# Performance work log

Hardware: AMD Instinct MI355X
Metric: run time of the kernel (lower is better)

Reference implementation:

```python
import jax, jax.numpy as jnp
import numpy as np

DIM = 2048
NH = 16
HD = DIM // NH
B = 2
S = 2048
HID = 5632  # multiple_of*ceil(int(2*4*dim/3)/multiple_of)
EPS = 1e-6


def setup_inputs() -> dict:
    key = jax.random.key(0)
    ks = jax.random.split(key, 9)
    sd = 0.02
    x = jax.random.normal(ks[0], (B, S, DIM), jnp.float32)
    wq = jax.random.normal(ks[1], (DIM, DIM), jnp.float32) * sd
    wk = jax.random.normal(ks[2], (DIM, DIM), jnp.float32) * sd
    wv = jax.random.normal(ks[3], (DIM, DIM), jnp.float32) * sd
    wo = jax.random.normal(ks[4], (DIM, DIM), jnp.float32) * sd
    w1 = jax.random.normal(ks[5], (DIM, HID), jnp.float32) * sd
    w2 = jax.random.normal(ks[6], (HID, DIM), jnp.float32) * sd
    w3 = jax.random.normal(ks[7], (DIM, HID), jnp.float32) * sd
    attn_norm_w = jnp.ones((DIM,), jnp.float32)
    ffn_norm_w = jnp.ones((DIM,), jnp.float32)
    # RoPE tables: freqs_cis = exp(i * t * theta_j), theta_j = 10000^(-2j/HD)
    inv_freq = 1.0 / (10000.0 ** (np.arange(0, HD, 2).astype(np.float32) / HD))
    t = np.arange(S, dtype=np.float32)
    ang = np.outer(t, inv_freq)  # [S, HD/2]
    freqs_cos = jnp.asarray(np.cos(ang), jnp.float32)
    freqs_sin = jnp.asarray(np.sin(ang), jnp.float32)
    # causal additive mask [1,1,S,S]
    mask = jnp.triu(jnp.full((S, S), float('-inf'), jnp.float32), k=1)[None, None]
    return dict(x=x, wq=wq, wk=wk, wv=wv, wo=wo, w1=w1, w2=w2, w3=w3,
                attn_norm_w=attn_norm_w, ffn_norm_w=ffn_norm_w,
                freqs_cos=freqs_cos, freqs_sin=freqs_sin, mask=mask)


def _rmsnorm(x, w):
    xf = x.astype(jnp.float32)
    v = jnp.mean(xf * xf, axis=-1, keepdims=True)
    return (xf * jax.lax.rsqrt(v + EPS)).astype(x.dtype) * w


def _rope(t, cos, sin):
    # t: [B,S,H,HD] -> pairs (re, im) on last dim
    tr = t.reshape(*t.shape[:-1], HD // 2, 2)
    re, im = tr[..., 0], tr[..., 1]
    c = cos[None, :, None, :]
    s = sin[None, :, None, :]
    out_re = re * c - im * s
    out_im = re * s + im * c
    return jnp.stack([out_re, out_im], axis=-1).reshape(t.shape)


def reference(x, wq, wk, wv, wo, w1, w2, w3, attn_norm_w, ffn_norm_w,
              freqs_cos, freqs_sin, mask):
    # --- attention sublayer ---
    h_in = _rmsnorm(x, attn_norm_w)
    xq = (h_in @ wq).reshape(B, S, NH, HD)
    xk = (h_in @ wk).reshape(B, S, NH, HD)
    xv = (h_in @ wv).reshape(B, S, NH, HD)
    xq = _rope(xq, freqs_cos, freqs_sin)
    xk = _rope(xk, freqs_cos, freqs_sin)
    scale = 1.0 / jnp.sqrt(jnp.float32(HD))
    scores = jnp.einsum('bqhd,bkhd->bhqk', xq, xk) * scale + mask
    probs = jax.nn.softmax(scores.astype(jnp.float32), axis=-1).astype(xq.dtype)
    attn = jnp.einsum('bhqk,bkhd->bqhd', probs, xv).reshape(B, S, DIM)
    h = x + attn @ wo
    # --- feedforward sublayer (SwiGLU) ---
    f_in = _rmsnorm(h, ffn_norm_w)
    ffn = (jax.nn.silu(f_in @ w1) * (f_in @ w3)) @ w2
    return h + ffn
```

## Files before the change

kernel.cpp:

```cpp
#include <hip/hip_runtime.h>

#define DIMQ 2048
#define NHQ  16
#define HDQ  128
#define BQ   2
#define SQ   2048
#define HIDQ 5632
#define MQ   (BQ * SQ)
#define SC_ATTN 0.08838834764831845f

using u16 = unsigned short;
using u32 = unsigned int;
typedef __attribute__((ext_vector_type(8))) short s16x8;
typedef __attribute__((ext_vector_type(4))) float f32x4;

__device__ __forceinline__ float bf2f(u16 v) {
  union { u32 u; float f; } w; w.u = ((u32)v) << 16; return w.f;
}
__device__ __forceinline__ u16 f2bf(float f) {
  union { float f; u32 u; } w; w.f = f;
  u32 r = w.u + 0x7FFFu + ((w.u >> 16) & 1u);
  return (u16)(r >> 16);
}

__device__ __forceinline__ f32x4 mfma16(s16x8 a, s16x8 b, f32x4 c) {
  return __builtin_amdgcn_mfma_f32_16x16x32_bf16(a, b, c, 0, 0, 0);
}

__device__ __forceinline__ void gl_lds16(const void* g, void* l) {
  __builtin_amdgcn_global_load_lds((const __attribute__((address_space(1))) void*)g,
                                   (__attribute__((address_space(3))) void*)l,
                                   16, 0, 0);
}

#define SBAR()                                   \
  {                                              \
    asm volatile("" ::: "memory");               \
    __builtin_amdgcn_s_barrier();                \
    asm volatile("" ::: "memory");               \
  }

__global__ __launch_bounds__(256) void transpose_cvt(const float* __restrict__ src,
                                                     u16* __restrict__ dst,
                                                     int R, int Cn) {
  __shared__ float tile[32][33];
  const int tx = threadIdx.x, ty = threadIdx.y;
  const int c0 = blockIdx.x * 32, r0 = blockIdx.y * 32;
#pragma unroll
  for (int i = 0; i < 4; ++i)
    tile[ty + i * 8][tx] = src[(size_t)(r0 + ty + i * 8) * Cn + c0 + tx];
  __syncthreads();
#pragma unroll
  for (int i = 0; i < 4; ++i)
    dst[(size_t)(c0 + ty + i * 8) * R + r0 + tx] = f2bf(tile[tx][ty + i * 8]);
}

__global__ __launch_bounds__(256) void transpose_cvt_ffn(const float* __restrict__ src,
                                                         u16* __restrict__ dst,
                                                         int base) {
  __shared__ float tile[32][33];
  const int tx = threadIdx.x, ty = threadIdx.y;
  const int c0 = blockIdx.x * 32, r0 = blockIdx.y * 32;
#pragma unroll
  for (int i = 0; i < 4; ++i)
    tile[ty + i * 8][tx] = src[(size_t)(r0 + ty + i * 8) * HIDQ + c0 + tx];
  __syncthreads();
#pragma unroll
  for (int i = 0; i < 4; ++i) {
    const int n = c0 + ty + i * 8;
    const int row = (n >> 7) * 256 + base + (n & 127);
    dst[(size_t)row * DIMQ + r0 + tx] = f2bf(tile[tx][ty + i * 8]);
  }
}

__global__ __launch_bounds__(256) void vtrans_k(const u16* __restrict__ qkv,
                                                u16* __restrict__ vt) {
  __shared__ u16 tile[32][33];
  const int bh = blockIdx.z;
  const int b = bh >> 4, h = bh & 15;
  const int s0 = blockIdx.x * 32, d0 = blockIdx.y * 32;
  const int tx = threadIdx.x, ty = threadIdx.y;
  const u16* src = qkv + (size_t)(b * SQ) * 6144 + 4096 + h * HDQ;
#pragma unroll
  for (int i = 0; i < 4; ++i)
    tile[ty + i * 8][tx] = src[(size_t)(s0 + ty + i * 8) * 6144 + d0 + tx];
  __syncthreads();
  u16* dst = vt + (size_t)bh * HDQ * SQ;
#pragma unroll
  for (int i = 0; i < 4; ++i)
    dst[(size_t)(d0 + ty + i * 8) * SQ + s0 + tx] = tile[tx][ty + i * 8];
}

__global__ __launch_bounds__(256) void rmsnorm_k(const float* __restrict__ x,
                                                 const float* __restrict__ w,
                                                 u16* __restrict__ o) {
  const int row = blockIdx.x;
  const int t = threadIdx.x;
  const float* xr = x + (size_t)row * DIMQ;
  const float4 a = ((const float4*)xr)[t * 2];
  const float4 b = ((const float4*)xr)[t * 2 + 1];
  float ss = a.x * a.x + a.y * a.y + a.z * a.z + a.w * a.w +
             b.x * b.x + b.y * b.y + b.z * b.z + b.w * b.w;
#pragma unroll
  for (int off = 32; off > 0; off >>= 1) ss += __shfl_down(ss, off);
  __shared__ float red[4];
  if ((t & 63) == 0) red[t >> 6] = ss;
  __syncthreads();
  ss = red[0] + red[1] + red[2] + red[3];
  const float rs = rsqrtf(ss * (1.0f / (float)DIMQ) + 1e-6f);
  const float4 wa = ((const float4*)w)[t * 2];
  const float4 wb = ((const float4*)w)[t * 2 + 1];
  s16x8 ov;
  ov[0] = (short)f2bf(a.x * rs * wa.x);
  ov[1] = (short)f2bf(a.y * rs * wa.y);
  ov[2] = (short)f2bf(a.z * rs * wa.z);
  ov[3] = (short)f2bf(a.w * rs * wa.w);
  ov[4] = (short)f2bf(b.x * rs * wb.x);
  ov[5] = (short)f2bf(b.y * rs * wb.y);
  ov[6] = (short)f2bf(b.z * rs * wb.z);
  ov[7] = (short)f2bf(b.w * rs * wb.w);
  *(s16x8*)(o + (size_t)row * DIMQ + t * 8) = ov;
}

template <int OM, int BN, int ROPE>
__global__ __launch_bounds__(512, 1) void gemm256(const u16* __restrict__ A,
                                                  const u16* __restrict__ Bt,
                                                  u16* __restrict__ Cb,
                                                  float* __restrict__ Cf,
                                                  const float* __restrict__ resid,
                                                  const float* __restrict__ fc,
                                                  const float* __restrict__ fs,
                                                  int N, int K, int lda) {
  constexpr int BT = BN * 128;
  constexpr int BLB = BN / 128;
  constexpr int WNv = (BN == 256) ? 4 : 2;
  constexpr int MF = (BN == 256) ? 8 : 4;
  constexpr int MFH = MF / 2;
  __shared__ u16 lds[(65536 + 2 * BT) / 2];
  const int tid = threadIdx.x, wid = tid >> 6, lane = tid & 63;
  const int wm = wid / WNv, wn = wid % WNv;
  const int r = lane & 15, kc = lane >> 4;
  const int nbx = N / BN;
  const int nwg = nbx << 4;
  const int o = blockIdx.x;
  const int seq = (o & 7) * (nwg >> 3) + (o >> 3);
  const int by = seq / nbx, bx = seq - by * nbx;
  const int m0 = by << 8, n0 = bx * BN;
  const int T = K >> 6;

  const u16* Ag = A + (size_t)m0 * lda;
  const u16* Bg = Bt + (size_t)n0 * K;

  const int pl = (tid * 16) ^ (((tid >> 3) & 7) << 4);
  const int prow = pl >> 7;
  const int pcol = (pl & 127) >> 1;

  const int rd0 = r * 128 + ((kc * 16) ^ ((r & 7) << 4));
  const int waveA = wm * (MF * 2048);
  const int waveB = wn * 8192;

  f32x4 acc[MF][4] = {};
  s16x8 af[MFH][2], bfL[2][2], bfH[2][2];

#define STAGE_A(G, kt, BUFB, h)                                                   \
  {                                                                               \
    _Pragma("unroll") for (int i = 0; i < 2; ++i)                                 \
        gl_lds16(G + (size_t)((h) * 128 + i * 64 + prow) * lda + (kt) * 64 + pcol,\
                 (char*)lds + (BUFB) + (h) * 16384 + i * 8192 + (wid << 10));     \
  }
#define STAGE_B(G, kt, BUFB, h)                                                   \
  {                                                                               \
    _Pragma("unroll") for (int i = 0; i < BLB; ++i)                               \
        gl_lds16(G + (size_t)((h) * (BN / 2) + i * 64 + prow) * K + (kt) * 64 + pcol, \
                 (char*)lds + (BUFB) + (h) * (BT / 2) + i * 8192 + (wid << 10));  \
  }

  STAGE_A(Ag, 0, 0, 0);
  STAGE_A(Ag, 0, 0, 1);
  STAGE_B(Bg, 0, 65536, 0);
  STAGE_B(Bg, 0, 65536, 1);
  STAGE_A(Ag, 1, 32768, 0);
  STAGE_A(Ag, 1, 32768, 1);
  asm volatile("s_waitcnt vmcnt(4)" ::: "memory");
  SBAR();

#define TILE_BODY(t, cur)                                                         \
  {                                                                               \
    const int tp1 = ((t) + 1 < T) ? (t) + 1 : T - 1;                              \
    const int tp2 = ((t) + 2 < T) ? (t) + 2 : T - 1;                              \
    const int AB = (cur)*32768;                                                   \
    const int BB = 65536 + (cur)*BT;                                              \
    const int BBn = 65536 + (1 - (cur)) * BT;                                     \
           \
    STAGE_B(Bg, tp1, BBn, 0);                                                     \
    _Pragma("unroll") for (int j = 0; j < MFH; ++j)                               \
        _Pragma("unroll") for (int ks = 0; ks < 2; ++ks)                          \
            af[j][ks] = *(const s16x8*)((const char*)lds + AB + waveA +           \
                                        j * 2048 + (rd0 ^ (ks << 6)));            \
    _Pragma("unroll") for (int n = 0; n < 2; ++n)                                 \
        _Pragma("unroll") for (int ks = 0; ks < 2; ++ks)                          \
            bfL[n][ks] = *(const s16x8*)((const char*)lds + BB + waveB +          \
                                         n * 2048 + (rd0 ^ (ks << 6)));           \
    __builtin_amdgcn_s_setprio(1);                                                \
    _Pragma("unroll") for (int ks = 0; ks < 2; ++ks)                              \
        _Pragma("unroll") for (int j = 0; j < MFH; ++j)                           \
            _Pragma("unroll") for (int n = 0; n < 2; ++n)                         \
                acc[j][n] = mfma16(af[j][ks], bfL[n][ks], acc[j][n]);             \
    __builtin_amdgcn_s_setprio(0);                                                \
                 \
    STAGE_B(Bg, tp1, BBn, 1);                                                     \
    _Pragma("unroll") for (int n = 0; n < 2; ++n)                                 \
        _Pragma("unroll") for (int ks = 0; ks < 2; ++ks)                          \
            bfH[n][ks] = *(const s16x8*)((const char*)lds + BB + waveB +          \
                                         (2 + n) * 2048 + (rd0 ^ (ks << 6)));     \
    __builtin_amdgcn_s_setprio(1);                                                \
    _Pragma("unroll") for (int ks = 0; ks < 2; ++ks)                              \
        _Pragma("unroll") for (int j = 0; j < MFH; ++j)                           \
            _Pragma("unroll") for (int n = 0; n < 2; ++n)                         \
                acc[j][2 + n] = mfma16(af[j][ks], bfH[n][ks], acc[j][2 + n]);     \
    __builtin_amdgcn_s_setprio(0);                                                \
                                  \
    _Pragma("unroll") for (int j = 0; j < MFH; ++j)                               \
        _Pragma("unroll") for (int ks = 0; ks < 2; ++ks)                          \
            af[j][ks] = *(const s16x8*)((const char*)lds + AB + waveA +           \
                                        (MFH + j) * 2048 + (rd0 ^ (ks << 6)));    \
    __builtin_amdgcn_s_setprio(1);                                                \
    _Pragma("unroll") for (int ks = 0; ks < 2; ++ks)                              \
        _Pragma("unroll") for (int j = 0; j < MFH; ++j)                           \
            _Pragma("unroll") for (int n = 0; n < 2; ++n)                         \
                acc[MFH + j][n] = mfma16(af[j][ks], bfL[n][ks], acc[MFH + j][n]); \
    __builtin_amdgcn_s_setprio(0);                                                \
    SBAR();     \
                  \
    STAGE_A(Ag, tp2, AB, 0);                                                      \
    STAGE_A(Ag, tp2, AB, 1);                                                      \
    __builtin_amdgcn_s_setprio(1);                                                \
    _Pragma("unroll") for (int ks = 0; ks < 2; ++ks)                              \
        _Pragma("unroll") for (int j = 0; j < MFH; ++j)                           \
            _Pragma("unroll") for (int n = 0; n < 2; ++n)                         \
                acc[MFH + j][2 + n] = mfma16(af[j][ks], bfH[n][ks], acc[MFH + j][2 + n]); \
    __builtin_amdgcn_s_setprio(0);                                                \
    asm volatile("s_waitcnt vmcnt(4)" ::: "memory");    \
    SBAR();                                                                       \
  }

  for (int tt = 0; tt < T; tt += 2) {
    TILE_BODY(tt, 0);
    TILE_BODY(tt + 1, 1);
  }
#undef TILE_BODY
#undef STAGE_A
#undef STAGE_B

  const bool do_rope = ROPE && (n0 < 4096);
#pragma unroll
  for (int mf = 0; mf < MF; ++mf)
#pragma unroll
    for (int nf = 0; nf < 4; ++nf)
#pragma unroll
      for (int j = 0; j < 4; ++j) {
        const int rr = m0 + wm * (MF * 16) + mf * 16 + kc * 4 + j;
        const int cc = n0 + wn * 64 + nf * 16 + r;
        float v = acc[mf][nf][j];
        if (OM == 0) {
          if (ROPE) {
            const float partner = __shfl_xor(v, 1);
            if (do_rope) {
              const int s = rr & (SQ - 1);
              const int i0 = (cc >> 1) & 63;
              const float cv = fc[s * 64 + i0];
              const float sv = fs[s * 64 + i0];
              v = ((r & 1) == 0) ? v * cv - partner * sv : v * cv + partner * sv;
            }
          }
          Cb[(size_t)rr * N + cc] = f2bf(v);
        } else {
          Cf[(size_t)rr * N + cc] = v + resid[(size_t)rr * N + cc];
        }
      }
}

__global__ __launch_bounds__(512, 1) void gemm_ffn(const u16* __restrict__ A,
                                                   const u16* __restrict__ Bi,
                                                   u16* __restrict__ act) {
  __shared__ u16 lds[65536];
  const int tid = threadIdx.x, wid = tid >> 6, lane = tid & 63;
  const int wm = wid >> 1, wn = wid & 1;
  const int r = lane & 15, kc = lane >> 4;
  const int o = blockIdx.x;
  const int seq = (o & 7) * 88 + (o >> 3);
  const int by = seq / 44, bx = seq - by * 44;
  const int m0 = by << 8;
  const int T = 32;

  const u16* Ag = A + (size_t)m0 * DIMQ;
  const u16* Bg = Bi + (size_t)bx * 256 * DIMQ;

  const int pl = (tid * 16) ^ (((tid >> 3) & 7) << 4);
  const int prow = pl >> 7, pcol = (pl & 127) >> 1;
  const int rd0 = r * 128 + ((kc * 16) ^ ((r & 7) << 4));
  const int waveA = wm * 8192;
  const int waveB = wn * 8192;

  f32x4 accG[4][4] = {}, accU[4][4] = {};
  s16x8 af[4][2], bL[2][2], bH[2][2];

#define STG(G, kt, BUFB, h)                                                       \
  {                                                                               \
    _Pragma("unroll") for (int i = 0; i < 2; ++i)                                 \
        gl_lds16(G + (size_t)((h) * 128 + i * 64 + prow) * DIMQ + (kt) * 64 + pcol,\
                 (char*)lds + (BUFB) + (h) * 16384 + i * 8192 + (wid << 10));     \
  }

  STG(Ag, 0, 0, 0);
  STG(Ag, 0, 0, 1);
  STG(Bg, 0, 65536, 0);
  STG(Bg, 0, 65536, 1);
  STG(Ag, 1, 32768, 0);
  STG(Ag, 1, 32768, 1);
  asm volatile("s_waitcnt vmcnt(4)" ::: "memory");
  SBAR();

#define FFN_BODY(t, cur)                                                          \
  {                                                                               \
    const int tp1 = ((t) + 1 < T) ? (t) + 1 : T - 1;                              \
    const int tp2 = ((t) + 2 < T) ? (t) + 2 : T - 1;                              \
    const int AB = (cur)*32768;                                                   \
    const int BB = 65536 + (cur)*32768;                                           \
    const int BBn = 65536 + (1 - (cur)) * 32768;                                  \
                            \
    STG(Bg, tp1, BBn, 0);                                                         \
    _Pragma("unroll") for (int j = 0; j < 4; ++j)                                 \
        _Pragma("unroll") for (int ks = 0; ks < 2; ++ks)                          \
            af[j][ks] = *(const s16x8*)((const char*)lds + AB + waveA +           \
                                        j * 2048 + (rd0 ^ (ks << 6)));            \
    _Pragma("unroll") for (int n = 0; n < 2; ++n)                                 \
        _Pragma("unroll") for (int ks = 0; ks < 2; ++ks)                          \
            bL[n][ks] = *(const s16x8*)((const char*)lds + BB + waveB +           \
                                        n * 2048 + (rd0 ^ (ks << 6)));            \
    __builtin_amdgcn_s_setprio(1);                                                \
    _Pragma("unroll") for (int ks = 0; ks < 2; ++ks)                              \
        _Pragma("unroll") for (int j = 0; j < 4; ++j)                             \
            _Pragma("unroll") for (int n = 0; n < 2; ++n)                         \
                accG[j][n] = mfma16(af[j][ks], bL[n][ks], accG[j][n]);            \
    __builtin_amdgcn_s_setprio(0);                                                \
                                 \
    STG(Bg, tp1, BBn, 1);                                                         \
    _Pragma("unroll") for (int n = 0; n < 2; ++n)                                 \
        _Pragma("unroll") for (int ks = 0; ks < 2; ++ks)                          \
            bH[n][ks] = *(const s16x8*)((const char*)lds + BB + waveB +           \
                                        (2 + n) * 2048 + (rd0 ^ (ks << 6)));      \
    __builtin_amdgcn_s_setprio(1);                                                \
    _Pragma("unroll") for (int ks = 0; ks < 2; ++ks)                              \
        _Pragma("unroll") for (int j = 0; j < 4; ++j)                             \
            _Pragma("unroll") for (int n = 0; n < 2; ++n)                         \
                accG[j][2 + n] = mfma16(af[j][ks], bH[n][ks], accG[j][2 + n]);    \
    __builtin_amdgcn_s_setprio(0);                                                \
                                                    \
    _Pragma("unroll") for (int n = 0; n < 2; ++n)                                 \
        _Pragma("unroll") for (int ks = 0; ks < 2; ++ks)                          \
            bL[n][ks] = *(const s16x8*)((const char*)lds + BB + 16384 + waveB +   \
                                        n * 2048 + (rd0 ^ (ks << 6)));            \
    __builtin_amdgcn_s_setprio(1);                                                \
    _Pragma("unroll") for (int ks = 0; ks < 2; ++ks)                              \
        _Pragma("unroll") for (int j = 0; j < 4; ++j)                             \
            _Pragma("unroll") for (int n = 0; n < 2; ++n)                         \
                accU[j][n] = mfma16(af[j][ks], bL[n][ks], accU[j][n]);            \
    __builtin_amdgcn_s_setprio(0);                                                \
                                                             \
    _Pragma("unroll") for (int n = 0; n < 2; ++n)                                 \
        _Pragma("unroll") for (int ks = 0; ks < 2; ++ks)                          \
            bH[n][ks] = *(const s16x8*)((const char*)lds + BB + 16384 + waveB +   \
                                        (2 + n) * 2048 + (rd0 ^ (ks << 6)));      \
    SBAR();                        \
                                                 \
    STG(Ag, tp2, AB, 0);                                                          \
    STG(Ag, tp2, AB, 1);                                                          \
    __builtin_amdgcn_s_setprio(1);                                                \
    _Pragma("unroll") for (int ks = 0; ks < 2; ++ks)                              \
        _Pragma("unroll") for (int j = 0; j < 4; ++j)                             \
            _Pragma("unroll") for (int n = 0; n < 2; ++n)                         \
                accU[j][2 + n] = mfma16(af[j][ks], bH[n][ks], accU[j][2 + n]);    \
    __builtin_amdgcn_s_setprio(0);                                                \
    asm volatile("s_waitcnt vmcnt(4)" ::: "memory");                              \
    SBAR();                                                                       \
  }

  for (int tt = 0; tt < T; tt += 2) {
    FFN_BODY(tt, 0);
    FFN_BODY(tt + 1, 1);
  }
#undef FFN_BODY
#undef STG

  const int cbase = bx * 128 + wn * 64;
#pragma unroll
  for (int mf = 0; mf < 4; ++mf)
#pragma unroll
    for (int nf = 0; nf < 4; ++nf)
#pragma unroll
      for (int j = 0; j < 4; ++j) {
        const int rr = m0 + wm * 64 + mf * 16 + kc * 4 + j;
        const int cc = cbase + nf * 16 + r;
        const float g = accG[mf][nf][j];
        const float u = accU[mf][nf][j];
        const float a = g / (1.f + __expf(-g)) * u;
        act[(size_t)rr * HIDQ + cc] = f2bf(a);
      }
}

__global__ __launch_bounds__(512) void attn_k(const u16* __restrict__ qkv,
                                              const u16* __restrict__ vt,
                                              u16* __restrict__ outb) {
  __shared__ u16 Kl[64 * 136];
  __shared__ u16 Vl[128 * 72];
  __shared__ u16 Pl[8][16 * 80];
  const int bh = blockIdx.x;
  const int pr = blockIdx.y;
  const int b = bh >> 4, h = bh & 15;
  const int tid = threadIdx.x, wid = tid >> 6, lane = tid & 63;
  const int r = lane & 15, kc = lane >> 4;
  const int nt_lo = pr + 1, nt = 32 - pr;
  const int qbase = ((wid < 4) ? pr * 64 : (31 - pr) * 64) + (wid & 3) * 16;
  const size_t base = (size_t)b * SQ * 6144;
  const u16* vtb = vt + (size_t)bh * HDQ * SQ;
  s16x8 qf[4];
  {
    const size_t qoff = base + (size_t)(qbase + r) * 6144 + h * HDQ;
#pragma unroll
    for (int kk = 0; kk < 4; ++kk)
      qf[kk] = *(const s16x8*)&qkv[qoff + kk * 32 + kc * 8];
  }
  f32x4 acc_o[8] = {};
  float m_run[4], l_run[4];
#pragma unroll
  for (int j = 0; j < 4; ++j) { m_run[j] = -1e30f; l_run[j] = 0.f; }
  const int kr = tid >> 4, kc8 = (tid & 15) * 8;
  const int vr = tid >> 3, vc8 = (tid & 7) * 8;
  const u16* kgp = &qkv[base + (size_t)kr * 6144 + 2048 + h * HDQ + kc8];
  const u16* vgp = &vtb[(size_t)vr * SQ + vc8];
  s16x8 kreg[2], vreg[2];
  kreg[0] = *(const s16x8*)kgp;
  kreg[1] = *(const s16x8*)(kgp + (size_t)32 * 6144);
  vreg[0] = *(const s16x8*)vgp;
  vreg[1] = *(const s16x8*)(vgp + (size_t)64 * SQ);
  for (int t = 0; t < nt; ++t) {
    const int kv0 = t * 64;
    __syncthreads();
    *(s16x8*)&Kl[kr * 136 + kc8] = kreg[0];
    *(s16x8*)&Kl[(kr + 32) * 136 + kc8] = kreg[1];
    *(s16x8*)&Vl[vr * 72 + vc8] = vreg[0];
    *(s16x8*)&Vl[(vr + 64) * 72 + vc8] = vreg[1];
    __syncthreads();
    if (t + 1 < nt) {
      const u16* kg = kgp + (size_t)(kv0 + 64) * 6144;
      const u16* vg = vgp + (kv0 + 64);
      kreg[0] = *(const s16x8*)kg;
      kreg[1] = *(const s16x8*)(kg + (size_t)32 * 6144);
      vreg[0] = *(const s16x8*)vg;
      vreg[1] = *(const s16x8*)(vg + (size_t)64 * SQ);
    }
    if (wid >= 4 || t < nt_lo) {
      f32x4 sacc[4] = {};
      __builtin_amdgcn_s_setprio(1);
#pragma unroll
      for (int nf = 0; nf < 4; ++nf)
#pragma unroll
        for (int kk = 0; kk < 4; ++kk) {
          const s16x8 kf = *(const s16x8*)&Kl[(nf * 16 + r) * 136 + kk * 32 + kc * 8];
          sacc[nf] = mfma16(qf[kk], kf, sacc[nf]);
        }
      __builtin_amdgcn_s_setprio(0);
      float p[4][4], alpha[4];
#pragma unroll
      for (int j = 0; j < 4; ++j) {
        const int qrow = qbase + kc * 4 + j;
        float svs[4];
        float tm = -1e30f;
#pragma unroll
        for (int nf = 0; nf < 4; ++nf) {
          const int key = kv0 + nf * 16 + r;
          float sv = sacc[nf][j] * SC_ATTN;
          sv = (key > qrow) ? -1e30f : sv;
          svs[nf] = sv;
          tm = fmaxf(tm, sv);
        }
        tm = fmaxf(tm, __shfl_xor(tm, 1));
        tm = fmaxf(tm, __shfl_xor(tm, 2));
        tm = fmaxf(tm, __shfl_xor(tm, 4));
        tm = fmaxf(tm, __shfl_xor(tm, 8));
        const float mnew = fmaxf(m_run[j], tm);
        alpha[j] = __expf(m_run[j] - mnew);
        m_run[j] = mnew;
        float rs = 0.f;
#pragma unroll
        for (int nf = 0; nf < 4; ++nf) {
          const float pv = __expf(svs[nf] - mnew);
          p[nf][j] = pv;
          rs += pv;
        }
        rs += __shfl_xor(rs, 1);
        rs += __shfl_xor(rs, 2);
        rs += __shfl_xor(rs, 4);
        rs += __shfl_xor(rs, 8);
        l_run[j] = l_run[j] * alpha[j] + rs;
      }
#pragma unroll
      for (int nf = 0; nf < 8; ++nf)
#pragma unroll
        for (int j = 0; j < 4; ++j)
          acc_o[nf][j] *= alpha[j];
#pragma unroll
      for (int nf = 0; nf < 4; ++nf)
#pragma unroll
        for (int j = 0; j < 4; ++j)
          Pl[wid][(kc * 4 + j) * 80 + nf * 16 + r] = f2bf(p[nf][j]);
      __builtin_amdgcn_s_setprio(1);
#pragma unroll
      for (int ks = 0; ks < 2; ++ks) {
        const s16x8 pa = *(const s16x8*)&Pl[wid][r * 80 + ks * 32 + kc * 8];
#pragma unroll
        for (int nf = 0; nf < 8; ++nf) {
          const s16x8 bv = *(const s16x8*)&Vl[(nf * 16 + r) * 72 + ks * 32 + kc * 8];
          acc_o[nf] = mfma16(pa, bv, acc_o[nf]);
        }
      }
      __builtin_amdgcn_s_setprio(0);
    }
  }
#pragma unroll
  for (int j = 0; j < 4; ++j) {
    const float inv = 1.0f / l_run[j];
    const size_t orow = (size_t)(b * SQ + qbase + kc * 4 + j) * DIMQ + h * HDQ;
#pragma unroll
    for (int nf = 0; nf < 8; ++nf)
      outb[orow + nf * 16 + r] = f2bf(acc_o[nf][j] * inv);
  }
}

extern "C" void kernel_launch(void* const* d_in, const int* in_sizes, int n_in,
                              void* d_out, int out_size, void* d_ws, size_t ws_size,
                              hipStream_t stream) {
  const float* x   = (const float*)d_in[0];
  const float* wq  = (const float*)d_in[1];
  const float* wk  = (const float*)d_in[2];
  const float* wv  = (const float*)d_in[3];
  const float* wo  = (const float*)d_in[4];
  const float* w1  = (const float*)d_in[5];
  const float* w2  = (const float*)d_in[6];
  const float* w3  = (const float*)d_in[7];
  const float* anw = (const float*)d_in[8];
  const float* fnw = (const float*)d_in[9];
  const float* fc  = (const float*)d_in[10];
  const float* fs  = (const float*)d_in[11];
  float* out = (float*)d_out;

  char* ws = (char*)d_ws;
  u16* wqkvT = (u16*)(ws);
  u16* woT   = (u16*)(ws + 25165824);
  u16* w13i  = (u16*)(ws + 25165824 + 8388608);
  u16* w2T   = (u16*)(ws + 25165824 + 8388608 + 46137344);
  u16* hin   = (u16*)(ws + 102760448);
  u16* qkvb  = (u16*)(ws + 119537664);
  u16* act   = qkvb;
  u16* attnb = (u16*)(ws + 119537664 + 50331648);
  u16* vtb   = (u16*)(ws + 119537664 + 50331648 + 16777216);
  float* h = out;

  const dim3 tb(32, 8);
  transpose_cvt<<<dim3(64, 64), tb, 0, stream>>>(wq, wqkvT, 2048, 2048);
  transpose_cvt<<<dim3(64, 64), tb, 0, stream>>>(wk, wqkvT + (size_t)2048 * 2048, 2048, 2048);
  transpose_cvt<<<dim3(64, 64), tb, 0, stream>>>(wv, wqkvT + (size_t)2 * 2048 * 2048, 2048, 2048);
  transpose_cvt<<<dim3(64, 64), tb, 0, stream>>>(wo, woT, 2048, 2048);
  transpose_cvt_ffn<<<dim3(176, 64), tb, 0, stream>>>(w1, w13i, 0);
  transpose_cvt_ffn<<<dim3(176, 64), tb, 0, stream>>>(w3, w13i, 128);
  transpose_cvt<<<dim3(64, 176), tb, 0, stream>>>(w2, w2T, 5632, 2048);

  rmsnorm_k<<<4096, 256, 0, stream>>>(x, anw, hin);
  gemm256<0, 128, 1><<<768, 512, 0, stream>>>(hin, wqkvT, qkvb, nullptr, nullptr, fc, fs, 6144, 2048, 2048);
  vtrans_k<<<dim3(64, 4, 32), tb, 0, stream>>>(qkvb, vtb);
  attn_k<<<dim3(32, 16), 512, 0, stream>>>(qkvb, vtb, attnb);
  gemm256<1, 128, 0><<<256, 512, 0, stream>>>(attnb, woT, nullptr, h, x, nullptr, nullptr, 2048, 2048, 2048);
  rmsnorm_k<<<4096, 256, 0, stream>>>(h, fnw, hin);
  gemm_ffn<<<704, 512, 0, stream>>>(hin, w13i, act);
  gemm256<1, 128, 0><<<256, 512, 0, stream>>>(act, w2T, nullptr, out, h, nullptr, nullptr, 2048, 5632, 5632);
}
```

Measured before the change: 633.7 us.

## Prefetch B tiles two iterations ahead alongside A in GEMM pipelines

Changes the B-operand staging in the generic GEMM and FFN GEMM kernels from one tile ahead to two tiles ahead, matching A. B loads are issued after the mid-tile barrier into the buffer just consumed, with an explicit lgkmcnt(0) wait added before that barrier, and the vmcnt waits are relaxed to keep more loads in flight. The aim is to hide global-load latency for B more fully. The cost is more outstanding memory operations and a dependence on the LDS reads finishing before the buffer is overwritten.

```diff
diff --git a/kernel.cpp b/kernel.cpp
--- a/kernel.cpp
+++ b/kernel.cpp
@@ -39,6 +39,7 @@
     __builtin_amdgcn_s_barrier();                \
     asm volatile("" ::: "memory");               \
   }
+#define LGKM0() asm volatile("s_waitcnt lgkmcnt(0)" ::: "memory")
 
 __global__ __launch_bounds__(256) void transpose_cvt(const float* __restrict__ src,
                                                      u16* __restrict__ dst,
@@ -174,6 +175,11 @@
         gl_lds16(G + (size_t)((h) * (BN / 2) + i * 64 + prow) * K + (kt) * 64 + pcol, \
                  (char*)lds + (BUFB) + (h) * (BT / 2) + i * 8192 + (wid << 10));  \
   }
+#define VMCNT_TILE()                                                              \
+  {                                                                               \
+    if (BN == 128) { asm volatile("s_waitcnt vmcnt(6)" ::: "memory"); }           \
+    else { asm volatile("s_waitcnt vmcnt(8)" ::: "memory"); }                     \
+  }
 
   STAGE_A(Ag, 0, 0, 0);
   STAGE_A(Ag, 0, 0, 1);
@@ -181,18 +187,17 @@
   STAGE_B(Bg, 0, 65536, 1);
   STAGE_A(Ag, 1, 32768, 0);
   STAGE_A(Ag, 1, 32768, 1);
-  asm volatile("s_waitcnt vmcnt(4)" ::: "memory");
+  STAGE_B(Bg, 1, 65536 + BT, 0);
+  STAGE_B(Bg, 1, 65536 + BT, 1);
+  VMCNT_TILE();
   SBAR();
 
 #define TILE_BODY(t, cur)                                                         \
   {                                                                               \
-    const int tp1 = ((t) + 1 < T) ? (t) + 1 : T - 1;                              \
     const int tp2 = ((t) + 2 < T) ? (t) + 2 : T - 1;                              \
     const int AB = (cur)*32768;                                                   \
     const int BB = 65536 + (cur)*BT;                                              \
-    const int BBn = 65536 + (1 - (cur)) * BT;                                     \
-           \
-    STAGE_B(Bg, tp1, BBn, 0);                                                     \
+                            \
     _Pragma("unroll") for (int j = 0; j < MFH; ++j)                               \
         _Pragma("unroll") for (int ks = 0; ks < 2; ++ks)                          \
             af[j][ks] = *(const s16x8*)((const char*)lds + AB + waveA +           \
@@ -207,8 +212,7 @@
             _Pragma("unroll") for (int n = 0; n < 2; ++n)                         \
                 acc[j][n] = mfma16(af[j][ks], bfL[n][ks], acc[j][n]);             \
     __builtin_amdgcn_s_setprio(0);                                                \
-                 \
-    STAGE_B(Bg, tp1, BBn, 1);                                                     \
+                                  \
     _Pragma("unroll") for (int n = 0; n < 2; ++n)                                 \
         _Pragma("unroll") for (int ks = 0; ks < 2; ++ks)                          \
             bfH[n][ks] = *(const s16x8*)((const char*)lds + BB + waveB +          \
@@ -230,17 +234,20 @@
             _Pragma("unroll") for (int n = 0; n < 2; ++n)                         \
                 acc[MFH + j][n] = mfma16(af[j][ks], bfL[n][ks], acc[MFH + j][n]); \
     __builtin_amdgcn_s_setprio(0);                                                \
-    SBAR();     \
-                  \
+    LGKM0();                             \
+    SBAR();                        \
+             \
     STAGE_A(Ag, tp2, AB, 0);                                                      \
     STAGE_A(Ag, tp2, AB, 1);                                                      \
+    STAGE_B(Bg, tp2, BB, 0);                                                      \
+    STAGE_B(Bg, tp2, BB, 1);                                                      \
     __builtin_amdgcn_s_setprio(1);                                                \
     _Pragma("unroll") for (int ks = 0; ks < 2; ++ks)                              \
         _Pragma("unroll") for (int j = 0; j < MFH; ++j)                           \
             _Pragma("unroll") for (int n = 0; n < 2; ++n)                         \
                 acc[MFH + j][2 + n] = mfma16(af[j][ks], bfH[n][ks], acc[MFH + j][2 + n]); \
     __builtin_amdgcn_s_setprio(0);                                                \
-    asm volatile("s_waitcnt vmcnt(4)" ::: "memory");    \
+    VMCNT_TILE();                 \
     SBAR();                                                                       \
   }
 
@@ -251,6 +258,7 @@
 #undef TILE_BODY
 #undef STAGE_A
 #undef STAGE_B
+#undef VMCNT_TILE
 
   const bool do_rope = ROPE && (n0 < 4096);
 #pragma unroll
@@ -318,18 +326,17 @@
   STG(Bg, 0, 65536, 1);
   STG(Ag, 1, 32768, 0);
   STG(Ag, 1, 32768, 1);
-  asm volatile("s_waitcnt vmcnt(4)" ::: "memory");
+  STG(Bg, 1, 98304, 0);
+  STG(Bg, 1, 98304, 1);
+  asm volatile("s_waitcnt vmcnt(8)" ::: "memory");
   SBAR();
 
 #define FFN_BODY(t, cur)                                                          \
   {                                                                               \
-    const int tp1 = ((t) + 1 < T) ? (t) + 1 : T - 1;                              \
     const int tp2 = ((t) + 2 < T) ? (t) + 2 : T - 1;                              \
     const int AB = (cur)*32768;                                                   \
     const int BB = 65536 + (cur)*32768;                                           \
-    const int BBn = 65536 + (1 - (cur)) * 32768;                                  \
-                            \
-    STG(Bg, tp1, BBn, 0);                                                         \
+                                            \
     _Pragma("unroll") for (int j = 0; j < 4; ++j)                                 \
         _Pragma("unroll") for (int ks = 0; ks < 2; ++ks)                          \
             af[j][ks] = *(const s16x8*)((const char*)lds + AB + waveA +           \
@@ -344,8 +351,7 @@
             _Pragma("unroll") for (int n = 0; n < 2; ++n)                         \
                 accG[j][n] = mfma16(af[j][ks], bL[n][ks], accG[j][n]);            \
     __builtin_amdgcn_s_setprio(0);                                                \
-                                 \
-    STG(Bg, tp1, BBn, 1);                                                         \
+                                                 \
     _Pragma("unroll") for (int n = 0; n < 2; ++n)                                 \
         _Pragma("unroll") for (int ks = 0; ks < 2; ++ks)                          \
             bH[n][ks] = *(const s16x8*)((const char*)lds + BB + waveB +           \
@@ -356,7 +362,7 @@
             _Pragma("unroll") for (int n = 0; n < 2; ++n)                         \
                 accG[j][2 + n] = mfma16(af[j][ks], bH[n][ks], accG[j][2 + n]);    \
     __builtin_amdgcn_s_setprio(0);                                                \
-                                                    \
+                                       \
     _Pragma("unroll") for (int n = 0; n < 2; ++n)                                 \
         _Pragma("unroll") for (int ks = 0; ks < 2; ++ks)                          \
             bL[n][ks] = *(const s16x8*)((const char*)lds + BB + 16384 + waveB +   \
@@ -367,22 +373,24 @@
             _Pragma("unroll") for (int n = 0; n < 2; ++n)                         \
                 accU[j][n] = mfma16(af[j][ks], bL[n][ks], accU[j][n]);            \
     __builtin_amdgcn_s_setprio(0);                                                \
-                                                             \
     _Pragma("unroll") for (int n = 0; n < 2; ++n)                                 \
         _Pragma("unroll") for (int ks = 0; ks < 2; ++ks)                          \
             bH[n][ks] = *(const s16x8*)((const char*)lds + BB + 16384 + waveB +   \
                                         (2 + n) * 2048 + (rd0 ^ (ks << 6)));      \
-    SBAR();                        \
-                                                 \
+    LGKM0();                    \
+    SBAR();                                                                       \
+                                 \
     STG(Ag, tp2, AB, 0);                                                          \
     STG(Ag, tp2, AB, 1);                                                          \
+    STG(Bg, tp2, BB, 0);                                                          \
+    STG(Bg, tp2, BB, 1);                                                          \
     __builtin_amdgcn_s_setprio(1);                                                \
     _Pragma("unroll") for (int ks = 0; ks < 2; ++ks)                              \
         _Pragma("unroll") for (int j = 0; j < 4; ++j)                             \
             _Pragma("unroll") for (int n = 0; n < 2; ++n)                         \
                 accU[j][2 + n] = mfma16(af[j][ks], bH[n][ks], accU[j][2 + n]);    \
     __builtin_amdgcn_s_setprio(0);                                                \
-    asm volatile("s_waitcnt vmcnt(4)" ::: "memory");                              \
+    asm volatile("s_waitcnt vmcnt(8)" ::: "memory");                              \
     SBAR();                                                                       \
   }
 
```

Result: slower. 649.5 us (+2.5%).

## Restructure attention softmax with transposed scores, exp2, lazy rescale, packed bf16 stores

Applied to the files above, without the earlier changes.

Computes the scores transposed (K·Q^T), so each lane holds one query row. Row max and sum then take two cross-lane shuffles instead of four per row, and only one running max/sum per lane is kept. The softmax scale and log2(e) are folded into Q at load time so exp2f can be used. Rescaling of the output accumulator is skipped unless the max grows by more than a threshold of 8. P is converted with packed v_cvt_pk_bf16 and written as 8-byte LDS stores. In exchange, Q is rounded to bf16 a second time after scaling, and the lazy-rescale threshold allows unnormalised exponentials up to 2^8, which could slightly change accuracy.

```diff
diff --git a/kernel.cpp b/kernel.cpp
--- a/kernel.cpp
+++ b/kernel.cpp
@@ -13,6 +13,7 @@
 using u32 = unsigned int;
 typedef __attribute__((ext_vector_type(8))) short s16x8;
 typedef __attribute__((ext_vector_type(4))) float f32x4;
+typedef __attribute__((ext_vector_type(2))) u32 u32x2;
 
 __device__ __forceinline__ float bf2f(u16 v) {
   union { u32 u; float f; } w; w.u = ((u32)v) << 16; return w.f;
@@ -21,6 +22,11 @@
   union { float f; u32 u; } w; w.f = f;
   u32 r = w.u + 0x7FFFu + ((w.u >> 16) & 1u);
   return (u16)(r >> 16);
+}
+__device__ __forceinline__ u32 cvtpk_bf16(float a, float b) {
+  u32 r;
+  asm("v_cvt_pk_bf16_f32 %0, %1, %2" : "=v"(r) : "v"(a), "v"(b));
+  return r;
 }
 
 __device__ __forceinline__ f32x4 mfma16(s16x8 a, s16x8 b, f32x4 c) {
@@ -39,6 +45,7 @@
     __builtin_amdgcn_s_barrier();                \
     asm volatile("" ::: "memory");               \
   }
+#define LGKM0() asm volatile("s_waitcnt lgkmcnt(0)" ::: "memory")
 
 __global__ __launch_bounds__(256) void transpose_cvt(const float* __restrict__ src,
                                                      u16* __restrict__ dst,
@@ -367,7 +374,7 @@
             _Pragma("unroll") for (int n = 0; n < 2; ++n)                         \
                 accU[j][n] = mfma16(af[j][ks], bL[n][ks], accU[j][n]);            \
     __builtin_amdgcn_s_setprio(0);                                                \
-                                                             \
+          \
     _Pragma("unroll") for (int n = 0; n < 2; ++n)                                 \
         _Pragma("unroll") for (int ks = 0; ks < 2; ++ks)                          \
             bH[n][ks] = *(const s16x8*)((const char*)lds + BB + 16384 + waveB +   \
@@ -422,19 +429,23 @@
   const int r = lane & 15, kc = lane >> 4;
   const int nt_lo = pr + 1, nt = 32 - pr;
   const int qbase = ((wid < 4) ? pr * 64 : (31 - pr) * 64) + (wid & 3) * 16;
+  const int qrow_r = qbase + r;
   const size_t base = (size_t)b * SQ * 6144;
   const u16* vtb = vt + (size_t)bh * HDQ * SQ;
   s16x8 qf[4];
   {
-    const size_t qoff = base + (size_t)(qbase + r) * 6144 + h * HDQ;
-#pragma unroll
-    for (int kk = 0; kk < 4; ++kk)
-      qf[kk] = *(const s16x8*)&qkv[qoff + kk * 32 + kc * 8];
+    const size_t qoff = base + (size_t)qrow_r * 6144 + h * HDQ;
+    const float QSC = SC_ATTN * 1.44269504f;
+#pragma unroll
+    for (int kk = 0; kk < 4; ++kk) {
+      s16x8 v = *(const s16x8*)&qkv[qoff + kk * 32 + kc * 8];
+#pragma unroll
+      for (int e = 0; e < 8; ++e) v[e] = (short)f2bf(bf2f((u16)v[e]) * QSC);
+      qf[kk] = v;
+    }
   }
   f32x4 acc_o[8] = {};
-  float m_run[4], l_run[4];
-#pragma unroll
-  for (int j = 0; j < 4; ++j) { m_run[j] = -1e30f; l_run[j] = 0.f; }
+  float m_run = -1e30f, l_run = 0.f;
   const int kr = tid >> 4, kc8 = (tid & 15) * 8;
   const int vr = tid >> 3, vc8 = (tid & 7) * 8;
   const u16* kgp = &qkv[base + (size_t)kr * 6144 + 2048 + h * HDQ + kc8];
@@ -461,60 +472,64 @@
       vreg[1] = *(const s16x8*)(vg + (size_t)64 * SQ);
     }
     if (wid >= 4 || t < nt_lo) {
-      f32x4 sacc[4] = {};
+      f32x4 st[4] = {};
       __builtin_amdgcn_s_setprio(1);
 #pragma unroll
       for (int nf = 0; nf < 4; ++nf)
 #pragma unroll
         for (int kk = 0; kk < 4; ++kk) {
           const s16x8 kf = *(const s16x8*)&Kl[(nf * 16 + r) * 136 + kk * 32 + kc * 8];
-          sacc[nf] = mfma16(qf[kk], kf, sacc[nf]);
+          st[nf] = mfma16(kf, qf[kk], st[nf]);
         }
       __builtin_amdgcn_s_setprio(0);
-      float p[4][4], alpha[4];
-#pragma unroll
-      for (int j = 0; j < 4; ++j) {
-        const int qrow = qbase + kc * 4 + j;
-        float svs[4];
-        float tm = -1e30f;
-#pragma unroll
-        for (int nf = 0; nf < 4; ++nf) {
-          const int key = kv0 + nf * 16 + r;
-          float sv = sacc[nf][j] * SC_ATTN;
-          sv = (key > qrow) ? -1e30f : sv;
-          svs[nf] = sv;
+      float pv[16];
+      float tm = -1e30f;
+#pragma unroll
+      for (int nf = 0; nf < 4; ++nf)
+#pragma unroll
+        for (int j = 0; j < 4; ++j) {
+          const int key = kv0 + nf * 16 + kc * 4 + j;
+          float sv = st[nf][j];
+          sv = (key > qrow_r) ? -1e30f : sv;
+          pv[nf * 4 + j] = sv;
           tm = fmaxf(tm, sv);
         }
-        tm = fmaxf(tm, __shfl_xor(tm, 1));
-        tm = fmaxf(tm, __shfl_xor(tm, 2));
-        tm = fmaxf(tm, __shfl_xor(tm, 4));
-        tm = fmaxf(tm, __shfl_xor(tm, 8));
-        const float mnew = fmaxf(m_run[j], tm);
-        alpha[j] = __expf(m_run[j] - mnew);
-        m_run[j] = mnew;
-        float rs = 0.f;
-#pragma unroll
-        for (int nf = 0; nf < 4; ++nf) {
-          const float pv = __expf(svs[nf] - mnew);
-          p[nf][j] = pv;
-          rs += pv;
+      tm = fmaxf(tm, __shfl_xor(tm, 16));
+      tm = fmaxf(tm, __shfl_xor(tm, 32));
+      if (__any(tm > m_run + 8.f)) {
+        const float mnew = fmaxf(m_run, tm);
+        const float alpha = exp2f(m_run - mnew);
+        m_run = mnew;
+        l_run *= alpha;
+#pragma unroll
+        for (int j = 0; j < 4; ++j) {
+          const float aj = __shfl(alpha, kc * 4 + j);
+#pragma unroll
+          for (int nf = 0; nf < 8; ++nf) acc_o[nf][j] *= aj;
         }
-        rs += __shfl_xor(rs, 1);
-        rs += __shfl_xor(rs, 2);
-        rs += __shfl_xor(rs, 4);
-        rs += __shfl_xor(rs, 8);
-        l_run[j] = l_run[j] * alpha[j] + rs;
       }
-#pragma unroll
-      for (int nf = 0; nf < 8; ++nf)
-#pragma unroll
-        for (int j = 0; j < 4; ++j)
-          acc_o[nf][j] *= alpha[j];
-#pragma unroll
-      for (int nf = 0; nf < 4; ++nf)
-#pragma unroll
-        for (int j = 0; j < 4; ++j)
-          Pl[wid][(kc * 4 + j) * 80 + nf * 16 + r] = f2bf(p[nf][j]);
+      float rs = 0.f;
+      u32 pk0[4], pk1[4];
+#pragma unroll
+      for (int nf = 0; nf < 4; ++nf) {
+        const float p0 = exp2f(pv[nf * 4 + 0] - m_run);
+        const float p1 = exp2f(pv[nf * 4 + 1] - m_run);
+        const float p2 = exp2f(pv[nf * 4 + 2] - m_run);
+        const float p3 = exp2f(pv[nf * 4 + 3] - m_run);
+        rs += (p0 + p1) + (p2 + p3);
+        pk0[nf] = cvtpk_bf16(p0, p1);
+        pk1[nf] = cvtpk_bf16(p2, p3);
+      }
+      rs += __shfl_xor(rs, 16);
+      rs += __shfl_xor(rs, 32);
+      l_run += rs;
+#pragma unroll
+      for (int nf = 0; nf < 4; ++nf) {
+        u32x2 w;
+        w[0] = pk0[nf];
+        w[1] = pk1[nf];
+        *(u32x2*)&Pl[wid][r * 80 + nf * 16 + kc * 4] = w;
+      }
       __builtin_amdgcn_s_setprio(1);
 #pragma unroll
       for (int ks = 0; ks < 2; ++ks) {
@@ -530,7 +545,8 @@
   }
 #pragma unroll
   for (int j = 0; j < 4; ++j) {
-    const float inv = 1.0f / l_run[j];
+    const float lj = __shfl(l_run, kc * 4 + j);
+    const float inv = 1.0f / lj;
     const size_t orow = (size_t)(b * SQ + qbase + kc * 4 + j) * DIMQ + h * HDQ;
 #pragma unroll
     for (int nf = 0; nf < 8; ++nf)
```

After: 593.7 us. 6.3% less time.
